# Optimization experiments

Hardware: AMD Instinct MI355X
Metric: run time of the kernel (lower is better)

The kernel has to match this reference:

```python
import jax, jax.numpy as jnp
import numpy as np

EPS = 1e-9
# exp factors for iterations i = 4,3,2,1,0,-1,-2 ; i == -2 -> 0.0
EXP_FACTORS = np.array([-(4.0 ** i) if i != -2 else 0.0 for i in range(4, -3, -1)], dtype=np.float32)


def setup_inputs() -> dict:
    key = jax.random.key(0)
    k1, k2 = jax.random.split(key)
    B, N, D = 16, 2048, 256
    preds = jax.random.normal(k1, (B, N, D), dtype=jnp.float32)
    labels = jax.random.normal(k2, (B, N, D), dtype=jnp.float32)
    return {"preds": preds, "labels": labels}


def _pairwise_dist(p1, p2):
    # [B,N,1] + [B,1,N] - 2 * p1 @ p2^T -> [B,N,N]
    p1_norm = jnp.sum(p1 * p1, axis=-1)[..., :, None]
    p2_norm = jnp.sum(p2 * p2, axis=-1)[..., None, :]
    return p1_norm + p2_norm - 2.0 * jnp.einsum('bnd,bmd->bnm', p1, p2)


def _approx_match(pwdist):
    B, N, _ = pwdist.shape
    match0 = jnp.zeros_like(pwdist)
    currency0 = jnp.ones((B, N, 1), dtype=pwdist.dtype)
    cost0 = jnp.ones((B, 1, N), dtype=pwdist.dtype)

    def body(carry, exp_factor):
        match, cost, currency = carry
        bids = jnp.exp(exp_factor * pwdist) * cost              # [B,N,N]
        bids = bids * currency / (jnp.sum(bids, axis=2, keepdims=True) + EPS)
        bid_wt = jnp.minimum(cost / (jnp.sum(bids, axis=1, keepdims=True) + EPS), 1.0)
        bids = bids * bid_wt
        match = match + bids
        cost = jnp.maximum(cost - jnp.sum(bids, axis=1, keepdims=True), 0.0)
        currency = jnp.maximum(currency - jnp.sum(bids, axis=2, keepdims=True), 0.0)
        return (match, cost, currency), None

    (match, _, _), _ = jax.lax.scan(body, (match0, cost0, currency0), jnp.asarray(EXP_FACTORS))
    return match


def reference(preds, labels):
    pwdist = _pairwise_dist(preds, labels)
    match = _approx_match(pwdist)
    return jnp.sum(match * pwdist)
```

## Files before the change

kernel.cpp:

```cpp
#include <hip/hip_runtime.h>
#include <cstdint>

#define B_ 16
#define N_ 2048
#define D_ 256
#define EPS_ 1e-9f

#define AS1 __attribute__((address_space(1)))
#define AS3 __attribute__((address_space(3)))

typedef float f4 __attribute__((ext_vector_type(4)));
typedef float f16v __attribute__((ext_vector_type(16)));
typedef int v8i __attribute__((ext_vector_type(8)));

__device__ float blockReduceSum(float x, float* red){
  int tid = threadIdx.x;
  red[tid] = x; __syncthreads();
  #pragma unroll
  for (int off = 128; off > 0; off >>= 1){
    if (tid < off) red[tid] += red[tid + off];
    __syncthreads();
  }
  float r = red[0]; __syncthreads();
  return r;
}

__global__ __launch_bounds__(256) void prep_kernel(
    const float* __restrict__ preds, const float* __restrict__ labels,
    unsigned char* __restrict__ pa8, unsigned char* __restrict__ pb8,
    float* __restrict__ pn, float* __restrict__ ln,
    float* __restrict__ cost, float* __restrict__ currency,
    int* __restrict__ dmin, float* __restrict__ Ppart,
    float* __restrict__ npart, float* __restrict__ out){
  int s = blockIdx.y;
  int tid = threadIdx.x;
  if (s == 0){
    int i = blockIdx.x * 256 + tid;
    if (i < B_ * N_){ cost[i] = 1.f; currency[i] = 1.f; }
    if (i < B_) dmin[i] = 0x7f7fffff;
    if (i == 0) out[0] = 0.f;
  }
  const float* src = s ? labels : preds;
  unsigned char* dst = s ? pb8 : pa8;
  float* norms = s ? ln : pn;
  int w = tid >> 6, lane = tid & 63;
  size_t row0 = (size_t)blockIdx.x * 16 + (size_t)w * 4;
  float4 v[4];
  #pragma unroll
  for (int q = 0; q < 4; q++)
    v[q] = ((const float4*)(src + (row0 + q) * D_))[lane];
  __shared__ f4 part[4][64];
  __shared__ float nred[4];
  f4 s4;
  s4[0] = v[0].x + v[1].x + v[2].x + v[3].x;
  s4[1] = v[0].y + v[1].y + v[2].y + v[3].y;
  s4[2] = v[0].z + v[1].z + v[2].z + v[3].z;
  s4[3] = v[0].w + v[1].w + v[2].w + v[3].w;
  float nsum = 0.f;
  #pragma unroll
  for (int q = 0; q < 4; q++){
    float sum = v[q].x*v[q].x + v[q].y*v[q].y + v[q].z*v[q].z + v[q].w*v[q].w;
    #pragma unroll
    for (int off = 32; off >= 1; off >>= 1) sum += __shfl_xor(sum, off);
    if (lane == 0){ norms[row0 + q] = sum; nsum += sum; }
    int pk = 0;
    pk = __builtin_amdgcn_cvt_pk_fp8_f32(v[q].x, v[q].y, pk, false);
    pk = __builtin_amdgcn_cvt_pk_fp8_f32(v[q].z, v[q].w, pk, true);
    ((unsigned int*)(dst + (row0 + q) * D_))[lane] = (unsigned int)pk;
  }
  part[w][lane] = s4;
  if (lane == 0) nred[w] = nsum;
  __syncthreads();
  if (tid < 64){
    f4 t = part[0][tid];
    #pragma unroll
    for (int q = 1; q < 4; q++){
      t[0] += part[q][tid][0]; t[1] += part[q][tid][1];
      t[2] += part[q][tid][2]; t[3] += part[q][tid][3];
    }
    *(f4*)(Ppart + ((size_t)s * 2048 + blockIdx.x) * 256 + tid * 4) = t;
  }
  if (tid == 0)
    npart[s * 2048 + blockIdx.x] = nred[0] + nred[1] + nred[2] + nred[3];
}

__global__ __launch_bounds__(512, 2) void gemm_minmax(
    const unsigned char* __restrict__ pa, const unsigned char* __restrict__ pbm,
    const float* __restrict__ pn, const float* __restrict__ ln,
    int* __restrict__ dmin)
{
  int lid = blockIdx.x;
  int xcd = lid & 7;
  int l = lid >> 3;
  int b = 2 * xcd + (l >> 4);
  int p = l & 15;
  int tn = (p & 7) * 256;
  int tmb = (p >> 3) * 1024;
  const unsigned char* A  = pa  + (size_t)b * N_ * D_;
  const unsigned char* Bm = pbm + (size_t)b * N_ * D_;
  __shared__ __align__(16) unsigned char Bs[256 * 256];
  __shared__ __align__(16) unsigned char As[2][128 * 256];
  __shared__ float minred[8];
  int tid = threadIdx.x, lane = tid & 63, w = tid >> 6;
  int wm = (w >> 2) * 64, wn = (w & 3) * 64;
  int l31 = lane & 31, half = lane >> 5;
  int rB = lane >> 4, cB = lane & 15;
  const int SC = 0x7F7F7F7F;

  #pragma unroll
  for (int q = 0; q < 8; q++){
    int R = q * 32 + w * 4;
    int r = R + rB;
    int gc = cB ^ (r & 7);
    __builtin_amdgcn_global_load_lds(
        (const AS1 unsigned int*)(const void*)&Bm[(size_t)(tn + r) * D_ + gc * 16],
        (AS3 unsigned int*)(void*)&Bs[R * 256 + lane * 16], 16, 0, 0);
  }
  #pragma unroll
  for (int q = 0; q < 4; q++){
    int R = q * 32 + w * 4;
    int r = R + rB;
    int gc = cB ^ (r & 7);
    __builtin_amdgcn_global_load_lds(
        (const AS1 unsigned int*)(const void*)&A[(size_t)(tmb + r) * D_ + gc * 16],
        (AS3 unsigned int*)(void*)&As[0][R * 256 + lane * 16], 16, 0, 0);
  }

  float lnj[2];
  #pragma unroll
  for (int j = 0; j < 2; j++)
    lnj[j] = ln[(size_t)b * N_ + tn + wn + j * 32 + l31];

  __syncthreads();

  v8i bfr[2][4];
  #pragma unroll
  for (int j = 0; j < 2; j++){
    int rb = wn + j * 32 + l31;
    #pragma unroll
    for (int kc = 0; kc < 4; kc++){
      int c0 = kc * 4 + half * 2;
      int4 lo = *(const int4*)&Bs[rb * 256 + ((c0 ^ (rb & 7)) * 16)];
      int4 hi = *(const int4*)&Bs[rb * 256 + (((c0 + 1) ^ (rb & 7)) * 16)];
      v8i t;
      t[0] = lo.x; t[1] = lo.y; t[2] = lo.z; t[3] = lo.w;
      t[4] = hi.x; t[5] = hi.y; t[6] = hi.z; t[7] = hi.w;
      bfr[j][kc] = t;
    }
  }

  float mind = 3.4e38f;
  int buf = 0;
  for (int step = 0; step < 8; step++){
    if (step < 7){
      #pragma unroll
      for (int q = 0; q < 4; q++){
        int R = q * 32 + w * 4;
        int r = R + rB;
        int gc = cB ^ (r & 7);
        __builtin_amdgcn_global_load_lds(
            (const AS1 unsigned int*)(const void*)&A[(size_t)(tmb + (step + 1) * 128 + r) * D_ + gc * 16],
            (AS3 unsigned int*)(void*)&As[buf ^ 1][R * 256 + lane * 16], 16, 0, 0);
      }
    }
    f16v acc[2][2];
    #pragma unroll
    for (int i = 0; i < 2; i++)
      #pragma unroll
      for (int j = 0; j < 2; j++) acc[i][j] = (f16v)0.f;

    #pragma unroll
    for (int kc = 0; kc < 4; kc++){
      v8i af[2];
      #pragma unroll
      for (int i = 0; i < 2; i++){
        int ra = wm + i * 32 + l31;
        int c0 = kc * 4 + half * 2;
        int4 lo = *(const int4*)&As[buf][ra * 256 + ((c0 ^ (ra & 7)) * 16)];
        int4 hi = *(const int4*)&As[buf][ra * 256 + (((c0 + 1) ^ (ra & 7)) * 16)];
        v8i t;
        t[0] = lo.x; t[1] = lo.y; t[2] = lo.z; t[3] = lo.w;
        t[4] = hi.x; t[5] = hi.y; t[6] = hi.z; t[7] = hi.w;
        af[i] = t;
      }
      #pragma unroll
      for (int i = 0; i < 2; i++)
        #pragma unroll
        for (int j = 0; j < 2; j++)
          acc[i][j] = __builtin_amdgcn_mfma_scale_f32_32x32x64_f8f6f4(
              af[i], bfr[j][kc], acc[i][j], 0, 0, 0, SC, 0, SC);
    }

    int tm = tmb + step * 128;
    #pragma unroll
    for (int i = 0; i < 2; i++){
      float4 pnq[4];
      #pragma unroll
      for (int q = 0; q < 4; q++)
        pnq[q] = *(const float4*)&pn[(size_t)b * N_ + tm + wm + i * 32 + half * 4 + q * 8];
      #pragma unroll
      for (int j = 0; j < 2; j++){
        #pragma unroll
        for (int reg = 0; reg < 16; reg++){
          float pv = ((const float*)&pnq[reg >> 2])[reg & 3];
          float v = pv + lnj[j] - 2.f * acc[i][j][reg];
          mind = fminf(mind, v);
        }
      }
    }
    if (step < 7) __syncthreads();
    buf ^= 1;
  }

  #pragma unroll
  for (int off = 32; off >= 1; off >>= 1) mind = fminf(mind, __shfl_xor(mind, off));
  if (lane == 0) minred[w] = mind;
  __syncthreads();
  if (tid == 0){
    float m = minred[0];
    #pragma unroll
    for (int q = 1; q < 8; q++) m = fminf(m, minred[q]);
    atomicMin(&dmin[b], __float_as_int(fmaxf(m, 0.f)));
  }
}

__global__ __launch_bounds__(256) void tail(
    const float* __restrict__ preds, const float* __restrict__ labels,
    const float* __restrict__ pn, const float* __restrict__ ln,
    float* __restrict__ cost, float* __restrict__ currency,
    const int* __restrict__ dmin, const float* __restrict__ Ppart,
    const float* __restrict__ npart, float* __restrict__ out)
{
  const float EF[6] = {-256.f, -64.f, -16.f, -4.f, -1.f, -0.25f};
  int b = blockIdx.x, tid = threadIdx.x;
  float dm = __int_as_float(dmin[b]);
  __shared__ float red[256];

  if (-0.25f * (dm - 16.f) < -55.f){
    float Pc = 0.f, Lc = 0.f;
    for (int k = 0; k < 128; k++){
      Pc += Ppart[((size_t)b * 128 + k) * 256 + tid];
      Lc += Ppart[((size_t)(2048 + b * 128 + k)) * 256 + tid];
    }
    float np = (tid < 128) ? npart[b * 128 + tid] : 0.f;
    float nl = (tid < 128) ? npart[2048 + b * 128 + tid] : 0.f;
    float Spn = blockReduceSum(np, red);
    float Sln = blockReduceSum(nl, red);
    float dot = blockReduceSum(Pc * Lc, red);
    if (tid == 0) atomicAdd(out, Spn + Sln - dot * (1.f / 1024.f));
    return;
  }

  __shared__ float alpha_l[N_];
  __shared__ float prow[D_];
  const float* A  = preds  + (size_t)b * N_ * D_;
  const float* Bm = labels + (size_t)b * N_ * D_;
  const float* pnb = pn + (size_t)b * N_;
  const float* lnb = ln + (size_t)b * N_;
  float* costb = cost + (size_t)b * N_;
  float* curb  = currency + (size_t)b * N_;
  for (int it = 0; it < 6; it++){
    float ef = EF[it];
    if (ef * (dm - 16.f) < -55.f) continue;
    float cost_c[8], colsum_c[8], bw_c[8], costnew_c[8];
    #pragma unroll
    for (int j = 0; j < 8; j++){ cost_c[j] = costb[j*256+tid]; colsum_c[j] = 0.f; }
    for (int r = 0; r < N_; r++){
      prow[tid] = A[(size_t)r * D_ + tid];
      __syncthreads();
      float s_c[8], rs = 0.f;
      for (int j = 0; j < 8; j++){
        int m = j*256+tid; float dot = 0.f;
        for (int k = 0; k < D_; k++) dot += prow[k] * Bm[(size_t)m * D_ + k];
        float d = pnb[r] + lnb[m] - 2.f*dot;
        float s = __expf(ef * d) * cost_c[j];
        s_c[j] = s; rs += s;
      }
      float tot = blockReduceSum(rs, red);
      float a = curb[r] / (tot + EPS_);
      if (tid == 0) alpha_l[r] = a;
      #pragma unroll
      for (int j = 0; j < 8; j++) colsum_c[j] += s_c[j] * a;
      __syncthreads();
    }
    #pragma unroll
    for (int j = 0; j < 8; j++){
      float cs = colsum_c[j];
      float bw = fminf(cost_c[j] / (cs + EPS_), 1.f);
      bw_c[j] = bw; costnew_c[j] = fmaxf(cost_c[j] - bw*cs, 0.f);
    }
    float contrib = 0.f;
    for (int r = 0; r < N_; r++){
      prow[tid] = A[(size_t)r * D_ + tid];
      __syncthreads();
      float a = alpha_l[r], rbs = 0.f;
      for (int j = 0; j < 8; j++){
        int m = j*256+tid; float dot = 0.f;
        for (int k = 0; k < D_; k++) dot += prow[k] * Bm[(size_t)m * D_ + k];
        float d = pnb[r] + lnb[m] - 2.f*dot;
        float bid = __expf(ef * d) * cost_c[j] * a * bw_c[j];
        rbs += bid; contrib += bid * d;
      }
      float tot = blockReduceSum(rbs, red);
      if (tid == 0) curb[r] = fmaxf(curb[r] - tot, 0.f);
      __syncthreads();
    }
    #pragma unroll
    for (int j = 0; j < 8; j++) costb[j*256+tid] = costnew_c[j];
    float ctot = blockReduceSum(contrib, red);
    if (tid == 0) atomicAdd(out, ctot);
    __syncthreads();
  }
  float s = 0.f;
  #pragma unroll
  for (int j = 0; j < 8; j++) s += costb[j*256+tid];
  float Sc = blockReduceSum(s, red);
  float sa = 0.f, spn = 0.f;
  #pragma unroll
  for (int j = 0; j < 8; j++){
    int i = j*256+tid;
    float a = curb[i] / (Sc + EPS_);
    alpha_l[i] = a; sa += a; spn += a * pnb[i];
  }
  float Sa  = blockReduceSum(sa, red);
  float Spn = blockReduceSum(spn, red);
  float Pc = 0.f;
  for (int r = 0; r < N_; r++)
    Pc += alpha_l[r] * A[(size_t)r * D_ + tid];
  __syncthreads();
  float sv = 0.f, sln = 0.f;
  #pragma unroll
  for (int j = 0; j < 8; j++){
    int i = j*256+tid;
    float c = costb[i];
    float bw = fminf(c / (c * Sa + EPS_), 1.f);
    float vv = c * bw;
    alpha_l[i] = vv; sv += vv; sln += vv * lnb[i];
  }
  float Sv  = blockReduceSum(sv, red);
  float Sln = blockReduceSum(sln, red);
  float Lc = 0.f;
  for (int m = 0; m < N_; m++)
    Lc += alpha_l[m] * Bm[(size_t)m * D_ + tid];
  float dot = blockReduceSum(Pc * Lc, red);
  if (tid == 0) atomicAdd(out, Spn * Sv + Sa * Sln - 2.f * dot);
}

extern "C" void kernel_launch(void* const* d_in, const int* in_sizes, int n_in,
                              void* d_out, int out_size, void* d_ws, size_t ws_size,
                              hipStream_t stream)
{
  const float* preds  = (const float*)d_in[0];
  const float* labels = (const float*)d_in[1];
  float* out = (float*)d_out;
  char* ws = (char*)d_ws;
  const size_t BN = (size_t)B_ * N_;
  size_t off = 0;
  float* cost     = (float*)(ws + off); off += BN * 4;
  float* currency = (float*)(ws + off); off += BN * 4;
  float* pn       = (float*)(ws + off); off += BN * 4;
  float* ln       = (float*)(ws + off); off += BN * 4;
  int*   dmin     = (int*)(ws + off);   off += 256;
  float* npart    = (float*)(ws + off); off += (size_t)2 * 2048 * 4;
  float* Ppart    = (float*)(ws + off); off += (size_t)2 * 2048 * 256 * 4;
  unsigned char* pa8 = (unsigned char*)(ws + off); off += BN * D_;
  unsigned char* pb8 = (unsigned char*)(ws + off); off += BN * D_;

  prep_kernel<<<dim3((unsigned)(BN / 16), 2), 256, 0, stream>>>(
      preds, labels, pa8, pb8, pn, ln, cost, currency, dmin, Ppart, npart, out);
  gemm_minmax<<<dim3(256), 512, 0, stream>>>(pa8, pb8, pn, ln, dmin);
  tail<<<dim3(B_), 256, 0, stream>>>(preds, labels, pn, ln, cost, currency, dmin,
                                     Ppart, npart, out);
}
```

Before: 126.2 us.

## Halve gemm_minmax tile height, reuse B smem for A buffers, double grid

Each gemm_minmax block now covers 512 rows instead of 1024 and each wave handles one 32-row MFMA tile, so the grid doubles to 512 blocks. After B fragments are loaded into registers, the B shared buffer is reused for the double-buffered A tiles and for row norms staged through LDS. This cuts LDS from 128KB to 64KB per block and raises launch bounds so more blocks fit per CU, aiming for better occupancy and latency hiding. The cost is that every B tile is loaded twice as often across the grid, and a sync is added at the top of each step.

After: 141.8 us. +12.4%, slower.

```diff
diff --git a/kernel.cpp b/kernel.cpp
--- a/kernel.cpp
+++ b/kernel.cpp
@@ -84,7 +84,7 @@
     npart[s * 2048 + blockIdx.x] = nred[0] + nred[1] + nred[2] + nred[3];
 }
 
-__global__ __launch_bounds__(512, 2) void gemm_minmax(
+__global__ __launch_bounds__(512, 4) void gemm_minmax(
     const unsigned char* __restrict__ pa, const unsigned char* __restrict__ pbm,
     const float* __restrict__ pn, const float* __restrict__ ln,
     int* __restrict__ dmin)
@@ -92,17 +92,20 @@
   int lid = blockIdx.x;
   int xcd = lid & 7;
   int l = lid >> 3;
-  int b = 2 * xcd + (l >> 4);
-  int p = l & 15;
+  int b = 2 * xcd + (l >> 5);
+  int p = l & 31;
   int tn = (p & 7) * 256;
-  int tmb = (p >> 3) * 1024;
+  int tmb = (p >> 3) * 512;
   const unsigned char* A  = pa  + (size_t)b * N_ * D_;
   const unsigned char* Bm = pbm + (size_t)b * N_ * D_;
-  __shared__ __align__(16) unsigned char Bs[256 * 256];
-  __shared__ __align__(16) unsigned char As[2][128 * 256];
+  __shared__ __align__(16) unsigned char smem[256 * 256];
   __shared__ float minred[8];
+  unsigned char* Bs = smem;
+  unsigned char* As0 = smem;
+  unsigned char* As1 = smem + 16384;
+  float* pnL = (float*)(smem + 32768);
   int tid = threadIdx.x, lane = tid & 63, w = tid >> 6;
-  int wm = (w >> 2) * 64, wn = (w & 3) * 64;
+  int wm = (w >> 2) * 32, wn = (w & 3) * 64;
   int l31 = lane & 31, half = lane >> 5;
   int rB = lane >> 4, cB = lane & 15;
   const int SC = 0x7F7F7F7F;
@@ -115,15 +118,6 @@
     __builtin_amdgcn_global_load_lds(
         (const AS1 unsigned int*)(const void*)&Bm[(size_t)(tn + r) * D_ + gc * 16],
         (AS3 unsigned int*)(void*)&Bs[R * 256 + lane * 16], 16, 0, 0);
-  }
-  #pragma unroll
-  for (int q = 0; q < 4; q++){
-    int R = q * 32 + w * 4;
-    int r = R + rB;
-    int gc = cB ^ (r & 7);
-    __builtin_amdgcn_global_load_lds(
-        (const AS1 unsigned int*)(const void*)&A[(size_t)(tmb + r) * D_ + gc * 16],
-        (AS3 unsigned int*)(void*)&As[0][R * 256 + lane * 16], 16, 0, 0);
   }
 
   float lnj[2];
@@ -149,66 +143,71 @@
     }
   }
 
+  __syncthreads();
+
+  __builtin_amdgcn_global_load_lds(
+      (const AS1 unsigned int*)(const void*)&pn[(size_t)b * N_ + tmb + tid],
+      (AS3 unsigned int*)(void*)&pnL[tid], 4, 0, 0);
+  #pragma unroll
+  for (int q = 0; q < 2; q++){
+    int R = q * 32 + w * 4;
+    int r = R + rB;
+    int gc = cB ^ (r & 7);
+    __builtin_amdgcn_global_load_lds(
+        (const AS1 unsigned int*)(const void*)&A[(size_t)(tmb + r) * D_ + gc * 16],
+        (AS3 unsigned int*)(void*)&As0[R * 256 + lane * 16], 16, 0, 0);
+  }
+
   float mind = 3.4e38f;
   int buf = 0;
   for (int step = 0; step < 8; step++){
+    __syncthreads();
+    unsigned char* Acur = buf ? As1 : As0;
+    unsigned char* Anxt = buf ? As0 : As1;
     if (step < 7){
       #pragma unroll
-      for (int q = 0; q < 4; q++){
+      for (int q = 0; q < 2; q++){
         int R = q * 32 + w * 4;
         int r = R + rB;
         int gc = cB ^ (r & 7);
         __builtin_amdgcn_global_load_lds(
-            (const AS1 unsigned int*)(const void*)&A[(size_t)(tmb + (step + 1) * 128 + r) * D_ + gc * 16],
-            (AS3 unsigned int*)(void*)&As[buf ^ 1][R * 256 + lane * 16], 16, 0, 0);
+            (const AS1 unsigned int*)(const void*)&A[(size_t)(tmb + (step + 1) * 64 + r) * D_ + gc * 16],
+            (AS3 unsigned int*)(void*)&Anxt[R * 256 + lane * 16], 16, 0, 0);
       }
     }
-    f16v acc[2][2];
-    #pragma unroll
-    for (int i = 0; i < 2; i++)
+    f16v acc[2];
+    acc[0] = (f16v)0.f; acc[1] = (f16v)0.f;
+
+    int ra = wm + l31;
+    #pragma unroll
+    for (int kc = 0; kc < 4; kc++){
+      int c0 = kc * 4 + half * 2;
+      int4 lo = *(const int4*)&Acur[ra * 256 + ((c0 ^ (ra & 7)) * 16)];
+      int4 hi = *(const int4*)&Acur[ra * 256 + (((c0 + 1) ^ (ra & 7)) * 16)];
+      v8i af;
+      af[0] = lo.x; af[1] = lo.y; af[2] = lo.z; af[3] = lo.w;
+      af[4] = hi.x; af[5] = hi.y; af[6] = hi.z; af[7] = hi.w;
       #pragma unroll
-      for (int j = 0; j < 2; j++) acc[i][j] = (f16v)0.f;
-
-    #pragma unroll
-    for (int kc = 0; kc < 4; kc++){
-      v8i af[2];
-      #pragma unroll
-      for (int i = 0; i < 2; i++){
-        int ra = wm + i * 32 + l31;
-        int c0 = kc * 4 + half * 2;
-        int4 lo = *(const int4*)&As[buf][ra * 256 + ((c0 ^ (ra & 7)) * 16)];
-        int4 hi = *(const int4*)&As[buf][ra * 256 + (((c0 + 1) ^ (ra & 7)) * 16)];
-        v8i t;
-        t[0] = lo.x; t[1] = lo.y; t[2] = lo.z; t[3] = lo.w;
-        t[4] = hi.x; t[5] = hi.y; t[6] = hi.z; t[7] = hi.w;
-        af[i] = t;
-      }
-      #pragma unroll
-      for (int i = 0; i < 2; i++)
-        #pragma unroll
-        for (int j = 0; j < 2; j++)
-          acc[i][j] = __builtin_amdgcn_mfma_scale_f32_32x32x64_f8f6f4(
-              af[i], bfr[j][kc], acc[i][j], 0, 0, 0, SC, 0, SC);
-    }
-
-    int tm = tmb + step * 128;
-    #pragma unroll
-    for (int i = 0; i < 2; i++){
-      float4 pnq[4];
-      #pragma unroll
-      for (int q = 0; q < 4; q++)
-        pnq[q] = *(const float4*)&pn[(size_t)b * N_ + tm + wm + i * 32 + half * 4 + q * 8];
+      for (int j = 0; j < 2; j++)
+        acc[j] = __builtin_amdgcn_mfma_scale_f32_32x32x64_f8f6f4(
+            af, bfr[j][kc], acc[j], 0, 0, 0, SC, 0, SC);
+    }
+
+    int prow0 = step * 64 + wm + half * 4;
+    #pragma unroll
+    for (int h = 0; h < 2; h++){
+      float4 p0 = *(const float4*)&pnL[prow0 + h * 16];
+      float4 p1 = *(const float4*)&pnL[prow0 + h * 16 + 8];
+      float pv[8] = {p0.x, p0.y, p0.z, p0.w, p1.x, p1.y, p1.z, p1.w};
       #pragma unroll
       for (int j = 0; j < 2; j++){
         #pragma unroll
-        for (int reg = 0; reg < 16; reg++){
-          float pv = ((const float*)&pnq[reg >> 2])[reg & 3];
-          float v = pv + lnj[j] - 2.f * acc[i][j][reg];
+        for (int r8 = 0; r8 < 8; r8++){
+          float v = pv[r8] + lnj[j] - 2.f * acc[j][h * 8 + r8];
           mind = fminf(mind, v);
         }
       }
     }
-    if (step < 7) __syncthreads();
     buf ^= 1;
   }
 
@@ -368,7 +367,7 @@
 
   prep_kernel<<<dim3((unsigned)(BN / 16), 2), 256, 0, stream>>>(
       preds, labels, pa8, pb8, pn, ln, cost, currency, dmin, Ppart, npart, out);
-  gemm_minmax<<<dim3(256), 512, 0, stream>>>(pa8, pb8, pn, ln, dmin);
+  gemm_minmax<<<dim3(512), 512, 0, stream>>>(pa8, pb8, pn, ln, dmin);
   tail<<<dim3(B_), 256, 0, stream>>>(preds, labels, pn, ln, cost, currency, dmin,
                                      Ppart, npart, out);
 }
```
